# Optimization experiments

Hardware: AMD Instinct MI355X
Metric: run time of the kernel (lower is better)

The kernel has to match this reference:

```python
import jax, jax.numpy as jnp
import numpy as np

THRESHOLD = 0.5
NEG_POS_RATIO = 3
ALPHA = 1.0
B, P, C, O = 64, 8732, 81, 32


def setup_inputs() -> dict:
    key = jax.random.key(0)
    k1, k2, k3, k4, k5, k6 = jax.random.split(key, 6)
    pred_locs = jax.random.normal(k1, (B, P, 4), dtype=jnp.float32)
    pred_scores = jax.random.normal(k2, (B, P, C), dtype=jnp.float32)
    # valid ground-truth corner boxes: sample center/size, convert to xy, clip to [0,1]
    ctr = jax.random.uniform(k3, (B, O, 2), minval=0.1, maxval=0.9)
    wh = jax.random.uniform(k4, (B, O, 2), minval=0.05, maxval=0.4)
    boxes = jnp.clip(jnp.concatenate([ctr - wh / 2, ctr + wh / 2], axis=-1), 0.0, 1.0)
    labels = jax.random.randint(k5, (B, O), 1, C, dtype=jnp.int64)
    pc = jax.random.uniform(k6, (P, 2), minval=0.05, maxval=0.95)
    pwh = jax.random.uniform(jax.random.fold_in(k6, 1), (P, 2), minval=0.05, maxval=0.3)
    priors_cxcy = jnp.concatenate([pc, pwh], axis=-1)
    return {"pred_locs": pred_locs, "pred_scores": pred_scores,
            "boxes": boxes, "labels": labels, "priors_cxcy": priors_cxcy}


def _jaccard(b, priors_xy):
    # b: [O,4] xy, priors_xy: [P,4] xy -> [O,P]
    lo = jnp.maximum(b[:, None, :2], priors_xy[None, :, :2])
    hi = jnp.minimum(b[:, None, 2:], priors_xy[None, :, 2:])
    inter = jnp.prod(jnp.clip(hi - lo, 0.0), axis=-1)
    area_b = jnp.prod(b[:, 2:] - b[:, :2], axis=-1)
    area_p = jnp.prod(priors_xy[:, 2:] - priors_xy[:, :2], axis=-1)
    return inter / (area_b[:, None] + area_p[None, :] - inter)


def _forward(pred_locs, pred_scores, boxes, labels, priors_cxcy):
    priors_xy = jnp.concatenate([priors_cxcy[:, :2] - priors_cxcy[:, 2:] / 2,
                                 priors_cxcy[:, :2] + priors_cxcy[:, 2:] / 2], axis=1)
    n_obj = boxes.shape[1]

    def match(b, l):
        ov = _jaccard(b, priors_xy)                      # [O,P]
        ov_fp = jnp.max(ov, axis=0)                      # [P]
        obj_fp = jnp.argmax(ov, axis=0)                  # [P]
        prior_fo = jnp.argmax(ov, axis=1)                # [O]
        obj_fp = obj_fp.at[prior_fo].set(jnp.arange(n_obj))
        ov_fp = ov_fp.at[prior_fo].set(1.0)
        lab = jnp.where(ov_fp < THRESHOLD, 0, l[obj_fp]) # [P]
        pt = b[obj_fp]                                   # [P,4] xy
        c = jnp.concatenate([(pt[:, 2:] + pt[:, :2]) / 2, pt[:, 2:] - pt[:, :2]], axis=1)
        g = jnp.concatenate([(c[:, :2] - priors_cxcy[:, :2]) / (priors_cxcy[:, 2:] / 10),
                             jnp.log(c[:, 2:] / priors_cxcy[:, 2:]) * 5], axis=1)
        return g, lab

    true_locs, true_classes = jax.vmap(match)(boxes, labels)  # [B,P,4], [B,P]

    pos = true_classes != 0                                   # [B,P]
    n_pos = jnp.sum(pos, axis=1)                              # [B]
    n_pos_total = jnp.sum(n_pos).astype(pred_locs.dtype)

    # L1Loss (mean over positive elements, 4 coords each)
    loc_abs = jnp.abs(pred_locs - true_locs) * pos[..., None].astype(pred_locs.dtype)
    loc_loss = jnp.sum(loc_abs) / (n_pos_total * 4.0)

    # per-prior cross entropy
    logp = jax.nn.log_softmax(pred_scores, axis=-1)           # [B,P,C]
    ce = -jnp.take_along_axis(logp, true_classes[..., None], axis=-1)[..., 0]  # [B,P]

    posf = pos.astype(ce.dtype)
    conf_pos_sum = jnp.sum(ce * posf)
    conf_neg = jnp.where(pos, 0.0, ce)
    conf_neg_sorted = -jnp.sort(-conf_neg, axis=1)            # descending
    ranks = jnp.arange(ce.shape[1])[None, :]
    hard = ranks < (NEG_POS_RATIO * n_pos)[:, None]
    conf_hard_neg_sum = jnp.sum(conf_neg_sorted * hard.astype(ce.dtype))

    conf_loss = (conf_hard_neg_sum + conf_pos_sum) / n_pos_total
    return conf_loss + ALPHA * loc_loss


def reference(pred_locs, pred_scores, boxes, labels, priors_cxcy):
    return _forward(pred_locs, pred_scores, boxes, labels, priors_cxcy)
```

## Files before the change

kernel.cpp:

```cpp
#include <hip/hip_runtime.h>

#define BB 64
#define PP 8732
#define OO 32
#define CC 81
#define NEGPOS 3
#define NCHUNK ((BB * PP) / 128)
#define NSL_A 18
#define NCH_B 32
#define CHB 273
#define NSL_C 8
#define SLC 1092

#define WS_POVFP  0
#define WS_BESTP  (WS_POVFP + BB*PP*8)
#define WS_LAB    (WS_BESTP + BB*NCH_B*OO*8)
#define WS_CENEG  (WS_LAB   + BB*PP*4)
#define WS_CEPOS  (WS_CENEG + BB*PP*4)
#define WS_LSUMB  (WS_CEPOS + NCHUNK*4)
#define WS_NPOSB  (WS_LSUMB + BB*NSL_C*4)
#define WS_HARDB  (WS_NPOSB + BB*NSL_C*4)

__global__ __launch_bounds__(512) void match_a(
    const float* __restrict__ boxes, const float* __restrict__ priors,
    unsigned long long* __restrict__ povfp)
{
    const int b = blockIdx.y;
    __shared__ float sbx[OO * 4];
    if (threadIdx.x < OO * 4) sbx[threadIdx.x] = boxes[b * OO * 4 + threadIdx.x];
    __syncthreads();
    const int p = blockIdx.x * 512 + threadIdx.x;
    if (p >= PP) return;

    float4 pr = ((const float4*)priors)[p];
    float plx = pr.x - pr.z * 0.5f, ply = pr.y - pr.w * 0.5f;
    float phx = pr.x + pr.z * 0.5f, phy = pr.y + pr.w * 0.5f;
    float parea = pr.z * pr.w;
    float bestv = -1.0f; int besto = 0;
#pragma unroll
    for (int o = 0; o < OO; ++o) {
        float b0 = sbx[o*4+0], b1 = sbx[o*4+1], b2 = sbx[o*4+2], b3 = sbx[o*4+3];
        float lox = fmaxf(b0, plx), loy = fmaxf(b1, ply);
        float hix = fminf(b2, phx), hiy = fminf(b3, phy);
        float inter = fmaxf(hix - lox, 0.0f) * fmaxf(hiy - loy, 0.0f);
        float iou = inter / ((b2 - b0) * (b3 - b1) + parea - inter);
        if (iou > bestv) { bestv = iou; besto = o; }
    }
    povfp[b * PP + p] = ((unsigned long long)__float_as_uint(bestv) << 32) | (unsigned)besto;
}

__global__ __launch_bounds__(256) void match_omax(
    const float* __restrict__ boxes, const float* __restrict__ priors,
    unsigned long long* __restrict__ bestp)
{
    const int b = blockIdx.y, ch = blockIdx.x, tid = threadIdx.x;
    const int o = tid & 31, sub = tid >> 5;
    const float b0 = boxes[(b*OO + o)*4 + 0], b1 = boxes[(b*OO + o)*4 + 1];
    const float b2 = boxes[(b*OO + o)*4 + 2], b3 = boxes[(b*OO + o)*4 + 3];
    const float barea = (b2 - b0) * (b3 - b1);
    const int base = ch * CHB;

    unsigned long long best = 0ull;
    for (int i = sub; i < CHB; i += 8) {
        int p = base + i;
        if (p >= PP) break;
        float4 pr = ((const float4*)priors)[p];
        float plx = pr.x - pr.z * 0.5f, ply = pr.y - pr.w * 0.5f;
        float phx = pr.x + pr.z * 0.5f, phy = pr.y + pr.w * 0.5f;
        float parea = pr.z * pr.w;
        float lox = fmaxf(b0, plx), loy = fmaxf(b1, ply);
        float hix = fminf(b2, phx), hiy = fminf(b3, phy);
        float inter = fmaxf(hix - lox, 0.0f) * fmaxf(hiy - loy, 0.0f);
        float iou = inter / (barea + parea - inter);
        unsigned long long enc =
            ((unsigned long long)__float_as_uint(iou) << 32) | (unsigned)(~(unsigned)p);
        best = (enc > best) ? enc : best;
    }
    unsigned long long w = __shfl_down(best, 32, 64);
    best = (w > best) ? w : best;
    __shared__ unsigned long long sred[4 * OO];
    if ((tid & 63) < 32) sred[(tid >> 6) * OO + o] = best;
    __syncthreads();
    if (tid < OO) {
        unsigned long long m = 0ull;
#pragma unroll
        for (int wv = 0; wv < 4; ++wv) {
            unsigned long long v = sred[wv * OO + tid];
            m = (v > m) ? v : m;
        }
        bestp[(b * NCH_B + ch) * OO + tid] = m;
    }
}

__global__ __launch_bounds__(256) void match_b(
    const float* __restrict__ pred_locs, const float* __restrict__ boxes,
    const int* __restrict__ labels, const float* __restrict__ priors,
    const unsigned long long* __restrict__ povfp,
    const unsigned long long* __restrict__ bestp,
    int* __restrict__ lab_out, int* __restrict__ npos_bs,
    float* __restrict__ lsum_bs)
{
    const int b = blockIdx.y, sl = blockIdx.x, tid = threadIdx.x;
    const int base = sl * SLC;
    __shared__ float sbx[OO * 4];
    __shared__ int   slab[OO];
    __shared__ int   spfo[OO];
    __shared__ signed char sovr[SLC];
    __shared__ float sredf[4];
    __shared__ int   sredi[4];

    if (tid < OO * 4) sbx[tid] = boxes[b * OO * 4 + tid];
    if (tid < OO)     slab[tid] = labels[b * OO + tid];
    if (tid < OO) {
        unsigned long long m = 0ull;
        for (int c = 0; c < NCH_B; ++c) {
            unsigned long long v = bestp[(b * NCH_B + c) * OO + tid];
            m = (v > m) ? v : m;
        }
        spfo[tid] = (int)(~(unsigned)(m & 0xFFFFFFFFull));
    }
    for (int i = tid; i < SLC; i += 256) sovr[i] = -1;
    __syncthreads();
    if (tid == 0) {
        for (int o = 0; o < OO; ++o) {
            int p = spfo[o] - base;
            if (p >= 0 && p < SLC) sovr[p] = (signed char)o;
        }
    }
    __syncthreads();

    float lsum = 0.0f; int lpos = 0;
    for (int i = tid; i < SLC; i += 256) {
        int p = base + i;
        if (p >= PP) break;
        unsigned long long pv = povfp[b * PP + p];
        int o = (int)(pv & 0xFFu);
        float ov = __uint_as_float((unsigned)(pv >> 32));
        int ovr = sovr[i];
        if (ovr >= 0) { o = ovr; ov = 1.0f; }
        int l = (ov < 0.5f) ? 0 : slab[o];
        lab_out[b * PP + p] = l;
        if (l != 0) {
            lpos++;
            float b0 = sbx[o*4+0], b1 = sbx[o*4+1], b2 = sbx[o*4+2], b3 = sbx[o*4+3];
            float4 pr = ((const float4*)priors)[p];
            float gx = ((b0 + b2) * 0.5f - pr.x) / (pr.z * 0.1f);
            float gy = ((b1 + b3) * 0.5f - pr.y) / (pr.w * 0.1f);
            float gw = logf((b2 - b0) / pr.z) * 5.0f;
            float gh = logf((b3 - b1) / pr.w) * 5.0f;
            float4 pl = ((const float4*)pred_locs)[b * PP + p];
            lsum += fabsf(pl.x - gx) + fabsf(pl.y - gy) + fabsf(pl.z - gw) + fabsf(pl.w - gh);
        }
    }
    for (int off = 32; off > 0; off >>= 1) {
        lsum += __shfl_down(lsum, off, 64);
        lpos += __shfl_down(lpos, off, 64);
    }
    if ((tid & 63) == 0) { sredf[tid >> 6] = lsum; sredi[tid >> 6] = lpos; }
    __syncthreads();
    if (tid == 0) {
        float s = 0.0f; int n = 0;
#pragma unroll
        for (int w = 0; w < 4; ++w) { s += sredf[w]; n += sredi[w]; }
        lsum_bs[b * NSL_C + sl] = s;
        npos_bs[b * NSL_C + sl] = n;
    }
}

__global__ __launch_bounds__(128) void ce_kernel(
    const float* __restrict__ scores, const int* __restrict__ lab,
    float* __restrict__ ce_neg, float* __restrict__ cepos)
{
    __shared__ float ss[128 * CC];
    const int tid = threadIdx.x;
    const int bp = blockIdx.x * 128 + tid;
    const int l = lab[bp];

    const float4* __restrict__ src =
        (const float4*)(scores + (long long)blockIdx.x * (128 * CC));
    float4* dst = (float4*)ss;
#pragma unroll 4
    for (int i = tid; i < (128 * CC) / 4; i += 128) dst[i] = src[i];
    __syncthreads();

    const float* v = ss + tid * CC;
    float m = v[0];
#pragma unroll
    for (int c = 1; c < CC; ++c) m = fmaxf(m, v[c]);
    float sum = 0.0f;
#pragma unroll
    for (int c = 0; c < CC; ++c) sum += __expf(v[c] - m);
    float lse = m + __logf(sum);
    float ce = lse - v[l];
    float pos = (l != 0) ? ce : 0.0f;
    ce_neg[bp] = (l != 0) ? 0.0f : ce;

    for (int off = 32; off > 0; off >>= 1) pos += __shfl_down(pos, off, 64);
    __shared__ float sr[2];
    if ((tid & 63) == 0) sr[tid >> 6] = pos;
    __syncthreads();
    if (tid == 0) cepos[blockIdx.x] = sr[0] + sr[1];
}

__global__ __launch_bounds__(512) void topk_kernel(
    const float* __restrict__ ce_neg, const int* __restrict__ npos_bs,
    float* __restrict__ hard_b)
{
    __shared__ float sv[PP];
    __shared__ int hist[256 * 16];
    __shared__ int chist[256];
    __shared__ unsigned sel[2];
    __shared__ float sr[8];
    __shared__ int sK;
    const int b = blockIdx.x, tid = threadIdx.x;
    for (int p = tid; p < PP; p += 512) sv[p] = ce_neg[b * PP + p];
    if (tid == 0) {
        int n = 0;
        for (int c = 0; c < NSL_C; ++c) n += npos_bs[b * NSL_C + c];
        int k = NEGPOS * n;
        sK = (k > PP) ? PP : k;
    }
    __syncthreads();
    const int K = sK;

    float hard = 0.0f;
    if (K > 0) {
        unsigned prefix = 0, mask = 0;
        unsigned remaining = (unsigned)K;
        for (int pass = 0; pass < 4; ++pass) {
            const int shift = 24 - 8 * pass;
            for (int i = tid; i < 256 * 16; i += 512) hist[i] = 0;
            __syncthreads();
            for (int p = tid; p < PP; p += 512) {
                unsigned u = __float_as_uint(sv[p]);
                if ((u & mask) == prefix)
                    atomicAdd(&hist[(((u >> shift) & 255) << 4) | (tid & 15)], 1);
            }
            __syncthreads();
            if (tid < 256) {
                int s = 0;
#pragma unroll
                for (int w = 0; w < 16; ++w) s += hist[(tid << 4) | w];
                chist[tid] = s;
            }
            __syncthreads();
            if (tid == 0) {
                unsigned cum = 0; int binsel = 0;
                for (int i = 255; i >= 0; --i) {
                    unsigned h = (unsigned)chist[i];
                    if (cum + h >= remaining) { binsel = i; break; }
                    cum += h;
                }
                sel[0] = (unsigned)binsel;
                sel[1] = remaining - cum;
            }
            __syncthreads();
            prefix |= sel[0] << shift;
            mask |= 0xFFu << shift;
            remaining = sel[1];
            __syncthreads();
        }
        float sgt = 0.0f;
        for (int p = tid; p < PP; p += 512) {
            unsigned u = __float_as_uint(sv[p]);
            if (u > prefix) sgt += sv[p];
        }
        for (int off = 32; off > 0; off >>= 1) sgt += __shfl_down(sgt, off, 64);
        if ((tid & 63) == 0) sr[tid >> 6] = sgt;
        __syncthreads();
        if (tid == 0) {
            hard = 0.0f;
#pragma unroll
            for (int w = 0; w < 8; ++w) hard += sr[w];
            hard += __uint_as_float(prefix) * (float)remaining;
        }
    }
    if (tid == 0) hard_b[b] = hard;
}

__global__ __launch_bounds__(256) void finalize_kernel(
    const float* __restrict__ cepos, const float* __restrict__ lsum_bs,
    const float* __restrict__ hard_b, const int* __restrict__ npos_bs,
    float* __restrict__ out)
{
    const int tid = threadIdx.x;
    float cpos = 0.0f, labs = 0.0f, chard = 0.0f; int n = 0;
    for (int i = tid; i < NCHUNK; i += 256) cpos += cepos[i];
    for (int i = tid; i < BB * NSL_C; i += 256) { labs += lsum_bs[i]; n += npos_bs[i]; }
    if (tid < BB) chard = hard_b[tid];
    for (int off = 32; off > 0; off >>= 1) {
        cpos  += __shfl_down(cpos, off, 64);
        labs  += __shfl_down(labs, off, 64);
        chard += __shfl_down(chard, off, 64);
        n     += __shfl_down(n, off, 64);
    }
    __shared__ float s0[4], s1[4], s2[4];
    __shared__ int s3[4];
    if ((tid & 63) == 0) { int w = tid >> 6; s0[w] = cpos; s1[w] = labs; s2[w] = chard; s3[w] = n; }
    __syncthreads();
    if (tid == 0) {
        float a = s0[0]+s0[1]+s0[2]+s0[3];
        float bsum = s1[0]+s1[1]+s1[2]+s1[3];
        float c = s2[0]+s2[1]+s2[2]+s2[3];
        float nf = (float)(s3[0]+s3[1]+s3[2]+s3[3]);
        out[0] = (c + a) / nf + bsum / (nf * 4.0f);
    }
}

extern "C" void kernel_launch(void* const* d_in, const int* in_sizes, int n_in,
                              void* d_out, int out_size, void* d_ws, size_t ws_size,
                              hipStream_t stream) {
    const float* pred_locs   = (const float*)d_in[0];
    const float* pred_scores = (const float*)d_in[1];
    const float* boxes       = (const float*)d_in[2];
    const int*   labels      = (const int*)d_in[3];
    const float* priors      = (const float*)d_in[4];
    float* out = (float*)d_out;

    char* ws = (char*)d_ws;
    unsigned long long* povfp = (unsigned long long*)(ws + WS_POVFP);
    unsigned long long* bestp = (unsigned long long*)(ws + WS_BESTP);
    int*   lab     = (int*)(ws + WS_LAB);
    float* ce_neg  = (float*)(ws + WS_CENEG);
    float* cepos   = (float*)(ws + WS_CEPOS);
    float* lsum_bs = (float*)(ws + WS_LSUMB);
    int*   nposbs  = (int*)(ws + WS_NPOSB);
    float* hard_b  = (float*)(ws + WS_HARDB);

    match_a<<<dim3(NSL_A, BB), 512, 0, stream>>>(boxes, priors, povfp);
    match_omax<<<dim3(NCH_B, BB), 256, 0, stream>>>(boxes, priors, bestp);
    match_b<<<dim3(NSL_C, BB), 256, 0, stream>>>(pred_locs, boxes, labels, priors,
                                                 povfp, bestp, lab, nposbs, lsum_bs);
    ce_kernel<<<NCHUNK, 128, 0, stream>>>(pred_scores, lab, ce_neg, cepos);
    topk_kernel<<<BB, 512, 0, stream>>>(ce_neg, nposbs, hard_b);
    finalize_kernel<<<1, 256, 0, stream>>>(cepos, lsum_bs, hard_b, nposbs, out);
}
```

Before: 358.4 us.

## Fuse match kernels and CE with matching; fold finalize into topk via ticket

Merges the per-prior IoU and per-object argmax kernels into one launch, and fuses label assignment and localization loss into the cross-entropy kernel. Labels are no longer written to and reread from global memory. The separate finalize launch is replaced by a last-block-done atomic ticket inside the top-k kernel. The serial cumulative histogram scan in top-k becomes a parallel suffix scan. This cuts launches and intermediate traffic, but the fused CE kernel now reduces 32 bestp chunks in every block and adds per-batch partial arrays.

```diff
diff --git a/kernel.cpp b/kernel.cpp
--- a/kernel.cpp
+++ b/kernel.cpp
@@ -5,109 +5,115 @@
 #define OO 32
 #define CC 81
 #define NEGPOS 3
-#define NCHUNK ((BB * PP) / 128)
 #define NSL_A 18
 #define NCH_B 32
 #define CHB 273
-#define NSL_C 8
-#define SLC 1092
+#define NCH_CE 69
 
 #define WS_POVFP  0
 #define WS_BESTP  (WS_POVFP + BB*PP*8)
-#define WS_LAB    (WS_BESTP + BB*NCH_B*OO*8)
-#define WS_CENEG  (WS_LAB   + BB*PP*4)
+#define WS_CENEG  (WS_BESTP + BB*NCH_B*OO*8)
 #define WS_CEPOS  (WS_CENEG + BB*PP*4)
-#define WS_LSUMB  (WS_CEPOS + NCHUNK*4)
-#define WS_NPOSB  (WS_LSUMB + BB*NSL_C*4)
-#define WS_HARDB  (WS_NPOSB + BB*NSL_C*4)
-
-__global__ __launch_bounds__(512) void match_a(
+#define WS_LSUMB  (WS_CEPOS + BB*NCH_CE*4)
+#define WS_NPOSB  (WS_LSUMB + BB*NCH_CE*4)
+#define WS_HARDB  (WS_NPOSB + BB*NCH_CE*4)
+#define WS_DONE   (WS_HARDB + BB*4)
+
+__global__ __launch_bounds__(512) void match_geom(
     const float* __restrict__ boxes, const float* __restrict__ priors,
-    unsigned long long* __restrict__ povfp)
+    unsigned long long* __restrict__ povfp, unsigned long long* __restrict__ bestp,
+    int* __restrict__ done)
 {
-    const int b = blockIdx.y;
+    const int b = blockIdx.y, gx = blockIdx.x, tid = threadIdx.x;
     __shared__ float sbx[OO * 4];
-    if (threadIdx.x < OO * 4) sbx[threadIdx.x] = boxes[b * OO * 4 + threadIdx.x];
-    __syncthreads();
-    const int p = blockIdx.x * 512 + threadIdx.x;
-    if (p >= PP) return;
-
-    float4 pr = ((const float4*)priors)[p];
-    float plx = pr.x - pr.z * 0.5f, ply = pr.y - pr.w * 0.5f;
-    float phx = pr.x + pr.z * 0.5f, phy = pr.y + pr.w * 0.5f;
-    float parea = pr.z * pr.w;
-    float bestv = -1.0f; int besto = 0;
-#pragma unroll
-    for (int o = 0; o < OO; ++o) {
-        float b0 = sbx[o*4+0], b1 = sbx[o*4+1], b2 = sbx[o*4+2], b3 = sbx[o*4+3];
-        float lox = fmaxf(b0, plx), loy = fmaxf(b1, ply);
-        float hix = fminf(b2, phx), hiy = fminf(b3, phy);
-        float inter = fmaxf(hix - lox, 0.0f) * fmaxf(hiy - loy, 0.0f);
-        float iou = inter / ((b2 - b0) * (b3 - b1) + parea - inter);
-        if (iou > bestv) { bestv = iou; besto = o; }
-    }
-    povfp[b * PP + p] = ((unsigned long long)__float_as_uint(bestv) << 32) | (unsigned)besto;
-}
-
-__global__ __launch_bounds__(256) void match_omax(
-    const float* __restrict__ boxes, const float* __restrict__ priors,
-    unsigned long long* __restrict__ bestp)
-{
-    const int b = blockIdx.y, ch = blockIdx.x, tid = threadIdx.x;
-    const int o = tid & 31, sub = tid >> 5;
-    const float b0 = boxes[(b*OO + o)*4 + 0], b1 = boxes[(b*OO + o)*4 + 1];
-    const float b2 = boxes[(b*OO + o)*4 + 2], b3 = boxes[(b*OO + o)*4 + 3];
-    const float barea = (b2 - b0) * (b3 - b1);
-    const int base = ch * CHB;
-
-    unsigned long long best = 0ull;
-    for (int i = sub; i < CHB; i += 8) {
-        int p = base + i;
-        if (p >= PP) break;
+    __shared__ unsigned long long sred[8 * OO];
+    if (tid < OO * 4) sbx[tid] = boxes[b * OO * 4 + tid];
+    if (gx == 0 && b == 0 && tid == 0) *done = 0;
+    __syncthreads();
+
+    if (gx < NSL_A) {
+        const int p = gx * 512 + tid;
+        if (p >= PP) return;
         float4 pr = ((const float4*)priors)[p];
         float plx = pr.x - pr.z * 0.5f, ply = pr.y - pr.w * 0.5f;
         float phx = pr.x + pr.z * 0.5f, phy = pr.y + pr.w * 0.5f;
         float parea = pr.z * pr.w;
-        float lox = fmaxf(b0, plx), loy = fmaxf(b1, ply);
-        float hix = fminf(b2, phx), hiy = fminf(b3, phy);
-        float inter = fmaxf(hix - lox, 0.0f) * fmaxf(hiy - loy, 0.0f);
-        float iou = inter / (barea + parea - inter);
-        unsigned long long enc =
-            ((unsigned long long)__float_as_uint(iou) << 32) | (unsigned)(~(unsigned)p);
-        best = (enc > best) ? enc : best;
-    }
-    unsigned long long w = __shfl_down(best, 32, 64);
-    best = (w > best) ? w : best;
-    __shared__ unsigned long long sred[4 * OO];
-    if ((tid & 63) < 32) sred[(tid >> 6) * OO + o] = best;
-    __syncthreads();
-    if (tid < OO) {
-        unsigned long long m = 0ull;
-#pragma unroll
-        for (int wv = 0; wv < 4; ++wv) {
-            unsigned long long v = sred[wv * OO + tid];
-            m = (v > m) ? v : m;
-        }
-        bestp[(b * NCH_B + ch) * OO + tid] = m;
+        float bestv = -1.0f; int besto = 0;
+#pragma unroll
+        for (int o = 0; o < OO; ++o) {
+            float b0 = sbx[o*4+0], b1 = sbx[o*4+1], b2 = sbx[o*4+2], b3 = sbx[o*4+3];
+            float lox = fmaxf(b0, plx), loy = fmaxf(b1, ply);
+            float hix = fminf(b2, phx), hiy = fminf(b3, phy);
+            float inter = fmaxf(hix - lox, 0.0f) * fmaxf(hiy - loy, 0.0f);
+            float iou = inter / ((b2 - b0) * (b3 - b1) + parea - inter);
+            if (iou > bestv) { bestv = iou; besto = o; }
+        }
+        povfp[b * PP + p] = ((unsigned long long)__float_as_uint(bestv) << 32) | (unsigned)besto;
+    } else {
+        const int ch = gx - NSL_A;
+        const int o = tid & 31, sub = tid >> 5;
+        const float b0 = sbx[o*4+0], b1 = sbx[o*4+1], b2 = sbx[o*4+2], b3 = sbx[o*4+3];
+        const float barea = (b2 - b0) * (b3 - b1);
+        const int base = ch * CHB;
+        unsigned long long best = 0ull;
+        for (int i = sub; i < CHB; i += 16) {
+            int p = base + i;
+            if (p >= PP) break;
+            float4 pr = ((const float4*)priors)[p];
+            float plx = pr.x - pr.z * 0.5f, ply = pr.y - pr.w * 0.5f;
+            float phx = pr.x + pr.z * 0.5f, phy = pr.y + pr.w * 0.5f;
+            float parea = pr.z * pr.w;
+            float lox = fmaxf(b0, plx), loy = fmaxf(b1, ply);
+            float hix = fminf(b2, phx), hiy = fminf(b3, phy);
+            float inter = fmaxf(hix - lox, 0.0f) * fmaxf(hiy - loy, 0.0f);
+            float iou = inter / (barea + parea - inter);
+            unsigned long long enc =
+                ((unsigned long long)__float_as_uint(iou) << 32) | (unsigned)(~(unsigned)p);
+            best = (enc > best) ? enc : best;
+        }
+        unsigned long long w = __shfl_down(best, 32, 64);
+        best = (w > best) ? w : best;
+        const int wid = tid >> 6, lane = tid & 63;
+        if (lane < 32) sred[wid * OO + o] = best;
+        __syncthreads();
+        if (tid < OO) {
+            unsigned long long m = 0ull;
+#pragma unroll
+            for (int wv = 0; wv < 8; ++wv) {
+                unsigned long long v = sred[wv * OO + tid];
+                m = (v > m) ? v : m;
+            }
+            bestp[(b * NCH_B + ch) * OO + tid] = m;
+        }
     }
 }
 
-__global__ __launch_bounds__(256) void match_b(
-    const float* __restrict__ pred_locs, const float* __restrict__ boxes,
-    const int* __restrict__ labels, const float* __restrict__ priors,
+__global__ __launch_bounds__(128) void ce_match(
+    const float* __restrict__ scores, const float* __restrict__ pred_locs,
+    const float* __restrict__ boxes, const int* __restrict__ labels,
+    const float* __restrict__ priors,
     const unsigned long long* __restrict__ povfp,
     const unsigned long long* __restrict__ bestp,
-    int* __restrict__ lab_out, int* __restrict__ npos_bs,
-    float* __restrict__ lsum_bs)
+    float* __restrict__ ce_neg, float* __restrict__ cepos,
+    float* __restrict__ lsum_bc, int* __restrict__ npos_bc)
 {
-    const int b = blockIdx.y, sl = blockIdx.x, tid = threadIdx.x;
-    const int base = sl * SLC;
+    __shared__ float ss[128 * CC];
     __shared__ float sbx[OO * 4];
     __shared__ int   slab[OO];
     __shared__ int   spfo[OO];
-    __shared__ signed char sovr[SLC];
-    __shared__ float sredf[4];
-    __shared__ int   sredi[4];
+    __shared__ signed char sovr[128];
+    __shared__ float srf[2], srl[2];
+    __shared__ int   sri[2];
+
+    const int b = blockIdx.y, ch = blockIdx.x, tid = threadIdx.x;
+    const int base = ch * 128;
+    const int nval = (PP - base < 128) ? (PP - base) : 128;
+
+    const float4* __restrict__ src =
+        (const float4*)(scores + ((long long)b * PP + base) * CC);
+    float4* dst = (float4*)ss;
+    const int n4 = (nval * CC) / 4;
+    for (int i = tid; i < n4; i += 128) dst[i] = src[i];
 
     if (tid < OO * 4) sbx[tid] = boxes[b * OO * 4 + tid];
     if (tid < OO)     slab[tid] = labels[b * OO + tid];
@@ -119,29 +125,38 @@
         }
         spfo[tid] = (int)(~(unsigned)(m & 0xFFFFFFFFull));
     }
-    for (int i = tid; i < SLC; i += 256) sovr[i] = -1;
+    sovr[tid] = -1;
     __syncthreads();
     if (tid == 0) {
         for (int o = 0; o < OO; ++o) {
             int p = spfo[o] - base;
-            if (p >= 0 && p < SLC) sovr[p] = (signed char)o;
-        }
-    }
-    __syncthreads();
-
-    float lsum = 0.0f; int lpos = 0;
-    for (int i = tid; i < SLC; i += 256) {
-        int p = base + i;
-        if (p >= PP) break;
+            if (p >= 0 && p < 128) sovr[p] = (signed char)o;
+        }
+    }
+    __syncthreads();
+
+    float pos = 0.0f, lsum = 0.0f; int lpos = 0;
+    if (tid < nval) {
+        const int p = base + tid;
+        const float* v = ss + tid * CC;
+        float m = v[0];
+#pragma unroll
+        for (int c = 1; c < CC; ++c) m = fmaxf(m, v[c]);
+        float sum = 0.0f;
+#pragma unroll
+        for (int c = 0; c < CC; ++c) sum += __expf(v[c] - m);
+        float lse = m + __logf(sum);
+
         unsigned long long pv = povfp[b * PP + p];
         int o = (int)(pv & 0xFFu);
         float ov = __uint_as_float((unsigned)(pv >> 32));
-        int ovr = sovr[i];
+        int ovr = sovr[tid];
         if (ovr >= 0) { o = ovr; ov = 1.0f; }
         int l = (ov < 0.5f) ? 0 : slab[o];
-        lab_out[b * PP + p] = l;
+        float ce = lse - v[l];
+        ce_neg[b * PP + p] = (l != 0) ? 0.0f : ce;
         if (l != 0) {
-            lpos++;
+            pos = ce; lpos = 1;
             float b0 = sbx[o*4+0], b1 = sbx[o*4+1], b2 = sbx[o*4+2], b3 = sbx[o*4+3];
             float4 pr = ((const float4*)priors)[p];
             float gx = ((b0 + b2) * 0.5f - pr.x) / (pr.z * 0.1f);
@@ -149,66 +164,31 @@
             float gw = logf((b2 - b0) / pr.z) * 5.0f;
             float gh = logf((b3 - b1) / pr.w) * 5.0f;
             float4 pl = ((const float4*)pred_locs)[b * PP + p];
-            lsum += fabsf(pl.x - gx) + fabsf(pl.y - gy) + fabsf(pl.z - gw) + fabsf(pl.w - gh);
+            lsum = fabsf(pl.x - gx) + fabsf(pl.y - gy) + fabsf(pl.z - gw) + fabsf(pl.w - gh);
         }
     }
     for (int off = 32; off > 0; off >>= 1) {
+        pos  += __shfl_down(pos, off, 64);
         lsum += __shfl_down(lsum, off, 64);
         lpos += __shfl_down(lpos, off, 64);
     }
-    if ((tid & 63) == 0) { sredf[tid >> 6] = lsum; sredi[tid >> 6] = lpos; }
-    __syncthreads();
-    if (tid == 0) {
-        float s = 0.0f; int n = 0;
-#pragma unroll
-        for (int w = 0; w < 4; ++w) { s += sredf[w]; n += sredi[w]; }
-        lsum_bs[b * NSL_C + sl] = s;
-        npos_bs[b * NSL_C + sl] = n;
+    if ((tid & 63) == 0) { int w = tid >> 6; srf[w] = pos; srl[w] = lsum; sri[w] = lpos; }
+    __syncthreads();
+    if (tid == 0) {
+        cepos[b * NCH_CE + ch]   = srf[0] + srf[1];
+        lsum_bc[b * NCH_CE + ch] = srl[0] + srl[1];
+        npos_bc[b * NCH_CE + ch] = sri[0] + sri[1];
     }
 }
 
-__global__ __launch_bounds__(128) void ce_kernel(
-    const float* __restrict__ scores, const int* __restrict__ lab,
-    float* __restrict__ ce_neg, float* __restrict__ cepos)
-{
-    __shared__ float ss[128 * CC];
-    const int tid = threadIdx.x;
-    const int bp = blockIdx.x * 128 + tid;
-    const int l = lab[bp];
-
-    const float4* __restrict__ src =
-        (const float4*)(scores + (long long)blockIdx.x * (128 * CC));
-    float4* dst = (float4*)ss;
-#pragma unroll 4
-    for (int i = tid; i < (128 * CC) / 4; i += 128) dst[i] = src[i];
-    __syncthreads();
-
-    const float* v = ss + tid * CC;
-    float m = v[0];
-#pragma unroll
-    for (int c = 1; c < CC; ++c) m = fmaxf(m, v[c]);
-    float sum = 0.0f;
-#pragma unroll
-    for (int c = 0; c < CC; ++c) sum += __expf(v[c] - m);
-    float lse = m + __logf(sum);
-    float ce = lse - v[l];
-    float pos = (l != 0) ? ce : 0.0f;
-    ce_neg[bp] = (l != 0) ? 0.0f : ce;
-
-    for (int off = 32; off > 0; off >>= 1) pos += __shfl_down(pos, off, 64);
-    __shared__ float sr[2];
-    if ((tid & 63) == 0) sr[tid >> 6] = pos;
-    __syncthreads();
-    if (tid == 0) cepos[blockIdx.x] = sr[0] + sr[1];
-}
-
 __global__ __launch_bounds__(512) void topk_kernel(
-    const float* __restrict__ ce_neg, const int* __restrict__ npos_bs,
-    float* __restrict__ hard_b)
+    const float* __restrict__ ce_neg, const int* __restrict__ npos_bc,
+    const float* __restrict__ cepos, const float* __restrict__ lsum_bc,
+    float* __restrict__ hard_b, int* __restrict__ done, float* __restrict__ out)
 {
     __shared__ float sv[PP];
     __shared__ int hist[256 * 16];
-    __shared__ int chist[256];
+    __shared__ int ssum[256];
     __shared__ unsigned sel[2];
     __shared__ float sr[8];
     __shared__ int sK;
@@ -216,7 +196,7 @@
     for (int p = tid; p < PP; p += 512) sv[p] = ce_neg[b * PP + p];
     if (tid == 0) {
         int n = 0;
-        for (int c = 0; c < NSL_C; ++c) n += npos_bs[b * NSL_C + c];
+        for (int c = 0; c < NCH_CE; ++c) n += npos_bc[b * NCH_CE + c];
         int k = NEGPOS * n;
         sK = (k > PP) ? PP : k;
     }
@@ -241,18 +221,20 @@
                 int s = 0;
 #pragma unroll
                 for (int w = 0; w < 16; ++w) s += hist[(tid << 4) | w];
-                chist[tid] = s;
-            }
-            __syncthreads();
-            if (tid == 0) {
-                unsigned cum = 0; int binsel = 0;
-                for (int i = 255; i >= 0; --i) {
-                    unsigned h = (unsigned)chist[i];
-                    if (cum + h >= remaining) { binsel = i; break; }
-                    cum += h;
-                }
-                sel[0] = (unsigned)binsel;
-                sel[1] = remaining - cum;
+                ssum[tid] = s;
+            }
+            __syncthreads();
+            for (int off = 1; off < 256; off <<= 1) {
+                int v = 0;
+                if (tid < 256) v = (tid + off < 256) ? ssum[tid + off] : 0;
+                __syncthreads();
+                if (tid < 256) ssum[tid] += v;
+                __syncthreads();
+            }
+            if (tid < 256 && (unsigned)ssum[tid] >= remaining &&
+                (tid == 255 || (unsigned)ssum[tid + 1] < remaining)) {
+                sel[0] = (unsigned)tid;
+                sel[1] = remaining - ((tid == 255) ? 0u : (unsigned)ssum[tid + 1]);
             }
             __syncthreads();
             prefix |= sel[0] << shift;
@@ -275,35 +257,38 @@
             hard += __uint_as_float(prefix) * (float)remaining;
         }
     }
-    if (tid == 0) hard_b[b] = hard;
-}
-
-__global__ __launch_bounds__(256) void finalize_kernel(
-    const float* __restrict__ cepos, const float* __restrict__ lsum_bs,
-    const float* __restrict__ hard_b, const int* __restrict__ npos_bs,
-    float* __restrict__ out)
-{
-    const int tid = threadIdx.x;
+    __shared__ int sticket;
+    if (tid == 0) {
+        hard_b[b] = hard;
+        __threadfence();
+        sticket = atomicAdd(done, 1);
+    }
+    __syncthreads();
+    if (sticket != BB - 1) return;
+
     float cpos = 0.0f, labs = 0.0f, chard = 0.0f; int n = 0;
-    for (int i = tid; i < NCHUNK; i += 256) cpos += cepos[i];
-    for (int i = tid; i < BB * NSL_C; i += 256) { labs += lsum_bs[i]; n += npos_bs[i]; }
-    if (tid < BB) chard = hard_b[tid];
+    for (int i = tid; i < BB * NCH_CE; i += 512) {
+        cpos += cepos[i];
+        labs += lsum_bc[i];
+        n    += npos_bc[i];
+    }
+    if (tid < BB) chard = atomicAdd(&hard_b[tid], 0.0f);
     for (int off = 32; off > 0; off >>= 1) {
         cpos  += __shfl_down(cpos, off, 64);
         labs  += __shfl_down(labs, off, 64);
         chard += __shfl_down(chard, off, 64);
         n     += __shfl_down(n, off, 64);
     }
-    __shared__ float s0[4], s1[4], s2[4];
-    __shared__ int s3[4];
-    if ((tid & 63) == 0) { int w = tid >> 6; s0[w] = cpos; s1[w] = labs; s2[w] = chard; s3[w] = n; }
-    __syncthreads();
-    if (tid == 0) {
-        float a = s0[0]+s0[1]+s0[2]+s0[3];
-        float bsum = s1[0]+s1[1]+s1[2]+s1[3];
-        float c = s2[0]+s2[1]+s2[2]+s2[3];
-        float nf = (float)(s3[0]+s3[1]+s3[2]+s3[3]);
-        out[0] = (c + a) / nf + bsum / (nf * 4.0f);
+    __shared__ float f0[8], f1[8], f2[8];
+    __shared__ int i3[8];
+    if ((tid & 63) == 0) { int w = tid >> 6; f0[w] = cpos; f1[w] = labs; f2[w] = chard; i3[w] = n; }
+    __syncthreads();
+    if (tid == 0) {
+        float a = 0.0f, bs = 0.0f, c = 0.0f; int nt = 0;
+#pragma unroll
+        for (int w = 0; w < 8; ++w) { a += f0[w]; bs += f1[w]; c += f2[w]; nt += i3[w]; }
+        float nf = (float)nt;
+        out[0] = (c + a) / nf + bs / (nf * 4.0f);
     }
 }
 
@@ -320,18 +305,16 @@
     char* ws = (char*)d_ws;
     unsigned long long* povfp = (unsigned long long*)(ws + WS_POVFP);
     unsigned long long* bestp = (unsigned long long*)(ws + WS_BESTP);
-    int*   lab     = (int*)(ws + WS_LAB);
     float* ce_neg  = (float*)(ws + WS_CENEG);
     float* cepos   = (float*)(ws + WS_CEPOS);
-    float* lsum_bs = (float*)(ws + WS_LSUMB);
-    int*   nposbs  = (int*)(ws + WS_NPOSB);
+    float* lsum_bc = (float*)(ws + WS_LSUMB);
+    int*   nposbc  = (int*)(ws + WS_NPOSB);
     float* hard_b  = (float*)(ws + WS_HARDB);
-
-    match_a<<<dim3(NSL_A, BB), 512, 0, stream>>>(boxes, priors, povfp);
-    match_omax<<<dim3(NCH_B, BB), 256, 0, stream>>>(boxes, priors, bestp);
-    match_b<<<dim3(NSL_C, BB), 256, 0, stream>>>(pred_locs, boxes, labels, priors,
-                                                 povfp, bestp, lab, nposbs, lsum_bs);
-    ce_kernel<<<NCHUNK, 128, 0, stream>>>(pred_scores, lab, ce_neg, cepos);
-    topk_kernel<<<BB, 512, 0, stream>>>(ce_neg, nposbs, hard_b);
-    finalize_kernel<<<1, 256, 0, stream>>>(cepos, lsum_bs, hard_b, nposbs, out);
+    int*   done    = (int*)(ws + WS_DONE);
+
+    match_geom<<<dim3(NSL_A + NCH_B, BB), 512, 0, stream>>>(boxes, priors, povfp, bestp, done);
+    ce_match<<<dim3(NCH_CE, BB), 128, 0, stream>>>(pred_scores, pred_locs, boxes, labels,
+                                                   priors, povfp, bestp,
+                                                   ce_neg, cepos, lsum_bc, nposbc);
+    topk_kernel<<<BB, 512, 0, stream>>>(ce_neg, nposbc, cepos, lsum_bc, hard_b, done, out);
 }
```

After: 364.7 us. Within noise of the previous version (+1.8%).
